# Kernel optimization log

Measured on AMD Instinct MI355X. Metric: run time of the kernel, lower is better.

Reference implementation:

```python
import jax, jax.numpy as jnp
import numpy as np
from jax import lax

R = 8  # REGION_NUM_

def _avgpool3(x):
    # AvgPool2d(kernel=H-2*(H//3), stride=H//3) -> exactly 3x3 spatial output
    H = x.shape[2]
    s = H // 3
    k = H - 2 * s
    y = lax.reduce_window(x, 0.0, lax.add, (1, 1, k, k), (1, 1, s, s), 'VALID')
    return y / float(k * k)

def _hist_drconv(x, hist, wa, ba, wb, bb, out_ch):
    # x: [B,Cin,H,W], hist: [B,R,H,W]
    B, Cin, H, W = x.shape
    p = _avgpool3(x)                                                     # [B,Cin,3,3]
    h = jax.nn.sigmoid(jnp.einsum('bchw,oc->bohw', p, wa) + ba[None, :, None, None])  # [B,R*R,3,3]
    hg = h.reshape(B, R, R, 3, 3)
    wbg = wb.reshape(R, Cin * out_ch, R)                                 # grouped 1x1 conv, groups=R
    kern = jnp.einsum('brchw,roc->brohw', hg, wbg) + bb.reshape(1, R, Cin * out_ch, 1, 1)
    ki = kern.reshape(B, R * out_ch, Cin, 3, 3)                          # per-sample dynamic kernels
    def per_sample(xi, kb):
        # xi: [Cin,H,W], kb: [R*out,Cin,3,3] -> [R*out,H,W]
        return lax.conv_general_dilated(xi[None], kb, (1, 1), [(1, 1), (1, 1)])[0]
    y = jax.vmap(per_sample)(x, ki)                                      # [B,R*out,H,W]
    y = y.reshape(B, R, out_ch, H, W)
    # asign_index: one-hot of argmax over regions, select-sum
    mask = jax.nn.one_hot(jnp.argmax(hist, axis=1), R, axis=1, dtype=y.dtype)  # [B,R,H,W]
    return (y * mask[:, :, None]).sum(axis=1)                            # [B,out,H,W]

def _bn_relu(y, g, b, m, v):
    scale = (g / jnp.sqrt(v + 1e-5))[None, :, None, None]
    return jax.nn.relu((y - m[None, :, None, None]) * scale + b[None, :, None, None])

def setup_inputs() -> dict:
    key = jax.random.key(0)
    ks = jax.random.split(key, 20)
    B, Cin, Cmid, Cout, H = 8, 8, 8, 8, 256
    f32 = jnp.float32
    d = {}
    d['x'] = jax.random.normal(ks[0], (B, Cin, H, H), f32)
    d['histmap'] = jax.random.uniform(ks[1], (B, R, H, H), dtype=f32)
    d['w1a'] = jax.random.normal(ks[2], (R * R, Cin), f32) * 0.1
    d['b1a'] = jax.random.normal(ks[3], (R * R,), f32) * 0.1
    d['w1b'] = jax.random.normal(ks[4], (R * Cin * Cmid, R), f32) * 0.1
    d['b1b'] = jax.random.normal(ks[5], (R * Cin * Cmid,), f32) * 0.1
    d['g1'] = jax.random.uniform(ks[6], (Cmid,), dtype=f32) + 0.5
    d['be1'] = jax.random.normal(ks[7], (Cmid,), f32) * 0.1
    d['m1'] = jax.random.normal(ks[8], (Cmid,), f32) * 0.1
    d['v1'] = jax.random.uniform(ks[9], (Cmid,), dtype=f32) + 0.5
    d['w2a'] = jax.random.normal(ks[10], (R * R, Cmid), f32) * 0.1
    d['b2a'] = jax.random.normal(ks[11], (R * R,), f32) * 0.1
    d['w2b'] = jax.random.normal(ks[12], (R * Cmid * Cout, R), f32) * 0.1
    d['b2b'] = jax.random.normal(ks[13], (R * Cmid * Cout,), f32) * 0.1
    d['g2'] = jax.random.uniform(ks[14], (Cout,), dtype=f32) + 0.5
    d['be2'] = jax.random.normal(ks[15], (Cout,), f32) * 0.1
    d['m2'] = jax.random.normal(ks[16], (Cout,), f32) * 0.1
    d['v2'] = jax.random.uniform(ks[17], (Cout,), dtype=f32) + 0.5
    return d

def reference(x, histmap, w1a, b1a, w1b, b1b, g1, be1, m1, v1,
              w2a, b2a, w2b, b2b, g2, be2, m2, v2):
    y = _hist_drconv(x, histmap, w1a, b1a, w1b, b1b, 8)
    y = _bn_relu(y, g1, be1, m1, v1)
    y = _hist_drconv(y, histmap, w2a, b2a, w2b, b2b, 8)
    return _bn_relu(y, g2, be2, m2, v2)
```

## Files before the change

kernel.cpp:

```cpp
#include <hip/hip_runtime.h>
#include <math.h>


#define HWPX 65536
#define HDIM 256

typedef __fp16 h2 __attribute__((ext_vector_type(2)));

#if defined(__has_builtin) && __has_builtin(__builtin_amdgcn_fdot2)
__device__ __forceinline__ float fdot2(h2 a, h2 b, float c) {
  return __builtin_amdgcn_fdot2(a, b, c, false);
}
#else
__device__ __forceinline__ float fdot2(h2 a, h2 b, float c) {
  return c + (float)a[0] * (float)b[0] + (float)a[1] * (float)b[1];
}
#endif

union UH { uint u; h2 h; };
union U4H { uint4 u4; h2 h[4]; };

__global__ __launch_bounds__(256) void prep_kernel(const float* __restrict__ x,
                                                   const float* __restrict__ hist,
                                                   float* __restrict__ rs1,
                                                   uint* __restrict__ xh,
                                                   unsigned char* __restrict__ regmap) {
  int u = blockIdx.x;
  int t = threadIdx.x;
  int wave = t >> 6, lane = t & 63;
  if (u < 2048) {
    int cp = u & 3, rg = (u >> 2) & 63, b = u >> 8;
    int row = rg * 4 + wave;
    const float* pa = x + ((size_t)(b * 8 + 2 * cp) * HWPX) + row * HDIM + lane * 4;
    const float4 va = *(const float4*)pa;
    const float4 vb = *(const float4*)(pa + HWPX);
    U4H pk;
    pk.h[0] = __builtin_amdgcn_cvt_pkrtz(va.x, vb.x);
    pk.h[1] = __builtin_amdgcn_cvt_pkrtz(va.y, vb.y);
    pk.h[2] = __builtin_amdgcn_cvt_pkrtz(va.z, vb.z);
    pk.h[3] = __builtin_amdgcn_cvt_pkrtz(va.w, vb.w);
    *(uint4*)(xh + (size_t)(b * 4 + cp) * HWPX + row * HDIM + lane * 4) = pk.u4;
    float a0 = 0.f, a1 = 0.f, a2 = 0.f, b0 = 0.f, b1 = 0.f, b2 = 0.f;
#pragma unroll
    for (int p = 0; p < 4; p++) {
      int px = lane * 4 + p;
      float fa = (&va.x)[p], fb = (&vb.x)[p];
      if (px <= 85)  { a0 += fa; b0 += fb; }
      if (px >= 85 && px <= 170) { a1 += fa; b1 += fb; }
      if (px >= 170) { a2 += fa; b2 += fb; }
    }
#pragma unroll
    for (int off = 32; off >= 1; off >>= 1) {
      a0 += __shfl_xor(a0, off); a1 += __shfl_xor(a1, off); a2 += __shfl_xor(a2, off);
      b0 += __shfl_xor(b0, off); b1 += __shfl_xor(b1, off); b2 += __shfl_xor(b2, off);
    }
    if (lane == 0) {
      float* qa = rs1 + ((size_t)(b * 8 + 2 * cp) * 256 + row) * 3;
      qa[0] = a0; qa[1] = a1; qa[2] = a2;
      float* qb = qa + 768;
      qb[0] = b0; qb[1] = b1; qb[2] = b2;
    }
  } else {
    int u2 = u - 2048;
    int b = u2 >> 6, rg = u2 & 63;
    int row = rg * 4 + wave;
    int x0 = lane * 4;
    const float* hp = hist + (size_t)b * 8 * HWPX + row * HDIM + x0;
    float4 hv[8];
#pragma unroll
    for (int r = 0; r < 8; r++) hv[r] = *(const float4*)(hp + (size_t)r * HWPX);
    uchar4 rg4;
#pragma unroll
    for (int p = 0; p < 4; p++) {
      float best = (&hv[0].x)[p];
      int reg = 0;
#pragma unroll
      for (int r = 1; r < 8; r++) {
        float q = (&hv[r].x)[p];
        if (q > best) { best = q; reg = r; }
      }
      (&rg4.x)[p] = (unsigned char)reg;
    }
    *(uchar4*)(regmap + (size_t)b * HWPX + row * HDIM + x0) = rg4;
  }
}

template <int LAYER>
__global__ __launch_bounds__(256) void conv_kernel(
    const uint* __restrict__ xh, const unsigned char* __restrict__ regmap,
    const float* __restrict__ rs,
    const float* __restrict__ wa, const float* __restrict__ ba,
    const float* __restrict__ wb, const float* __restrict__ bb,
    const float* __restrict__ g, const float* __restrict__ be,
    const float* __restrict__ m, const float* __restrict__ v,
    uint* __restrict__ outh, float* __restrict__ outf,
    float* __restrict__ rs2out) {
  __shared__ uint KsU[8 * 292];
  __shared__ float pp[72][3];
  __shared__ float pP[8][9];
  __shared__ float hh[576];
  __shared__ float bns[8], bnsh[8];

  int bid = blockIdx.x;
  int b = bid & 7;
  int rg = bid >> 3;
  int wave = threadIdx.x >> 6, lane = threadIdx.x & 63;
  int row = rg * 4 + wave;
  int x0 = lane * 4;
  int t = threadIdx.x;

  if (t < 216) {
    int u = t / 3, part = t - 3 * (t / 3);
    int c = u / 9, ij = u % 9, i = ij / 3, j = ij % 3;
    int r0 = 85 * i + part * 29;
    int cnt = (part == 2) ? 28 : 29;
    const float* q = rs + ((size_t)(b * 8 + c) * 256 + r0) * 3 + j;
    float s = 0.f;
    for (int k = 0; k < cnt; k++) s += q[k * 3];
    pp[u][part] = s;
  }
  if (t >= 248) {
    int oc = t - 248;
    float s = g[oc] * rsqrtf(v[oc] + 1e-5f);
    bns[oc] = s;
    bnsh[oc] = be[oc] - m[oc] * s;
  }
  __syncthreads();
  if (t < 72) pP[t / 9][t % 9] = (pp[t][0] + pp[t][1] + pp[t][2]) * (1.f / 7396.f);
  __syncthreads();
  for (int u = t; u < 576; u += 256) {
    int o = u / 9, ij = u - o * 9;
    float z = ba[o];
#pragma unroll
    for (int c = 0; c < 8; c++) z += pP[c][ij] * wa[o * 8 + c];
    hh[u] = 1.f / (1.f + expf(-z));
  }
  __syncthreads();
  {
    int reg = t >> 5, z = t & 31, oc = z >> 2, q = z & 3;
    int row0 = reg * 64 + oc * 8 + q * 2;
    const float* w0p = wb + row0 * 8;
    float4 wA  = *(const float4*)(w0p);
    float4 wA2 = *(const float4*)(w0p + 4);
    float4 wB  = *(const float4*)(w0p + 8);
    float4 wB2 = *(const float4*)(w0p + 12);
    float bb0 = bb[row0], bb1 = bb[row0 + 1];
    const float* hp = hh + reg * 72;
#pragma unroll
    for (int tap = 0; tap < 9; tap++) {
      float v0 = bb0, v1 = bb1;
#pragma unroll
      for (int cc = 0; cc < 4; cc++) {
        float hv = hp[cc * 9 + tap];
        v0 += hv * (&wA.x)[cc];
        v1 += hv * (&wB.x)[cc];
      }
#pragma unroll
      for (int cc = 0; cc < 4; cc++) {
        float hv = hp[(4 + cc) * 9 + tap];
        v0 += hv * (&wA2.x)[cc];
        v1 += hv * (&wB2.x)[cc];
      }
      UH pk;
      pk.h[0] = (__fp16)v0;
      pk.h[1] = (__fp16)v1;
      KsU[reg * 292 + tap * 32 + z] = pk.u;
    }
  }
  __syncthreads();

  uint win[4][3][6];
#pragma unroll
  for (int cp = 0; cp < 4; cp++) {
    const uint* plane = xh + (size_t)(b * 4 + cp) * HWPX;
#pragma unroll
    for (int dy = 0; dy < 3; dy++) {
      int yy = row + dy - 1;
      if ((unsigned)yy < 256u) {
        const uint* rp = plane + yy * HDIM + x0;
        uint4 mv = *(const uint4*)rp;
        win[cp][dy][0] = (x0 > 0) ? rp[-1] : 0u;
        win[cp][dy][1] = mv.x; win[cp][dy][2] = mv.y;
        win[cp][dy][3] = mv.z; win[cp][dy][4] = mv.w;
        win[cp][dy][5] = (x0 < 252) ? rp[4] : 0u;
      } else {
#pragma unroll
        for (int q = 0; q < 6; q++) win[cp][dy][q] = 0u;
      }
    }
  }

  uchar4 rg4 = *(const uchar4*)(regmap + (size_t)b * HWPX + row * HDIM + x0);

  float acc[4][8];
#pragma unroll
  for (int p = 0; p < 4; p++)
#pragma unroll
    for (int oc = 0; oc < 8; oc++) acc[p][oc] = 0.f;

#pragma unroll
  for (int p = 0; p < 4; p++) {
    int reg = (&rg4.x)[p];
    const char* Kr = (const char*)KsU + reg * 1168;
#pragma unroll
    for (int di = 0; di < 3; di++) {
#pragma unroll
      for (int dj = 0; dj < 3; dj++) {
        UH w0, w1, w2, w3;
        w0.u = win[0][di][p + dj];
        w1.u = win[1][di][p + dj];
        w2.u = win[2][di][p + dj];
        w3.u = win[3][di][p + dj];
        const char* kt = Kr + (di * 3 + dj) * 128;
#pragma unroll
        for (int oc = 0; oc < 8; oc++) {
          U4H kw;
          kw.u4 = *(const uint4*)(kt + oc * 16);
          float a = acc[p][oc];
          a = fdot2(w0.h, kw.h[0], a);
          a = fdot2(w1.h, kw.h[1], a);
          a = fdot2(w2.h, kw.h[2], a);
          a = fdot2(w3.h, kw.h[3], a);
          acc[p][oc] = a;
        }
      }
    }
  }

#pragma unroll
  for (int p = 0; p < 4; p++)
#pragma unroll
    for (int oc = 0; oc < 8; oc++)
      acc[p][oc] = fmaxf(acc[p][oc] * bns[oc] + bnsh[oc], 0.f);

  if (LAYER == 1) {
#pragma unroll
    for (int cp = 0; cp < 4; cp++) {
      U4H pk;
#pragma unroll
      for (int p = 0; p < 4; p++)
        pk.h[p] = __builtin_amdgcn_cvt_pkrtz(acc[p][2 * cp], acc[p][2 * cp + 1]);
      *(uint4*)(outh + (size_t)(b * 4 + cp) * HWPX + row * HDIM + x0) = pk.u4;
    }
#pragma unroll
    for (int oc = 0; oc < 8; oc++) {
      float s0 = 0.f, s1 = 0.f, s2 = 0.f;
#pragma unroll
      for (int p = 0; p < 4; p++) {
        int px = x0 + p;
        float val = acc[p][oc];
        if (px <= 85) s0 += val;
        if (px >= 85 && px <= 170) s1 += val;
        if (px >= 170) s2 += val;
      }
#pragma unroll
      for (int off = 32; off >= 1; off >>= 1) {
        s0 += __shfl_xor(s0, off);
        s1 += __shfl_xor(s1, off);
        s2 += __shfl_xor(s2, off);
      }
      if (lane == 0) {
        float* q = rs2out + ((size_t)(b * 8 + oc) * 256 + row) * 3;
        q[0] = s0; q[1] = s1; q[2] = s2;
      }
    }
  } else {
#pragma unroll
    for (int oc = 0; oc < 8; oc++) {
      float4 o4 = make_float4(acc[0][oc], acc[1][oc], acc[2][oc], acc[3][oc]);
      *(float4*)(outf + (size_t)(b * 8 + oc) * HWPX + row * HDIM + x0) = o4;
    }
  }
}

extern "C" void kernel_launch(void* const* d_in, const int* in_sizes, int n_in,
                              void* d_out, int out_size, void* d_ws, size_t ws_size,
                              hipStream_t stream) {
  const float* x    = (const float*)d_in[0];
  const float* hist = (const float*)d_in[1];
  const float* w1a  = (const float*)d_in[2];
  const float* b1a  = (const float*)d_in[3];
  const float* w1b  = (const float*)d_in[4];
  const float* b1b  = (const float*)d_in[5];
  const float* g1   = (const float*)d_in[6];
  const float* be1  = (const float*)d_in[7];
  const float* m1   = (const float*)d_in[8];
  const float* v1   = (const float*)d_in[9];
  const float* w2a  = (const float*)d_in[10];
  const float* b2a  = (const float*)d_in[11];
  const float* w2b  = (const float*)d_in[12];
  const float* b2b  = (const float*)d_in[13];
  const float* g2   = (const float*)d_in[14];
  const float* be2  = (const float*)d_in[15];
  const float* m2   = (const float*)d_in[16];
  const float* v2   = (const float*)d_in[17];
  float* outp = (float*)d_out;

  char* ws = (char*)d_ws;
  unsigned char* regmap = (unsigned char*)ws;
  uint* xh  = (uint*)(ws + 524288);
  uint* y1h = (uint*)(ws + 8912896);
  float* rs1 = (float*)(ws + 17301504);
  float* rs2 = (float*)(ws + 17399808);

  prep_kernel<<<2560, 256, 0, stream>>>(x, hist, rs1, xh, regmap);
  conv_kernel<1><<<512, 256, 0, stream>>>(xh, regmap, rs1, w1a, b1a, w1b, b1b,
                                          g1, be1, m1, v1, y1h, nullptr, rs2);
  conv_kernel<2><<<512, 256, 0, stream>>>(y1h, regmap, rs2, w2a, b2a, w2b, b2b,
                                          g2, be2, m2, v2, nullptr, outp, nullptr);
}
```

Before: 55.72 us.

## Fuse fp16 packing and region argmax into first conv kernel

The fp32-to-fp16 packing of x and the histogram argmax move out of the prep kernel into the first conv kernel, which now reads x and hist directly and writes the region map. The prep kernel shrinks to just the row-sum pass, removing the xh intermediate buffer round trip through memory. Global loads in conv1 are issued before the dynamic-kernel generation so they can overlap with it. The cost is that conv1 reads x as fp32, including halo rows, which is more traffic per block, and it carries more register pressure from the extra loads.

New measurement: 58.96 us. 1.06x slower.

```diff
diff --git a/kernel.cpp b/kernel.cpp
--- a/kernel.cpp
+++ b/kernel.cpp
@@ -20,81 +20,47 @@
 union UH { uint u; h2 h; };
 union U4H { uint4 u4; h2 h[4]; };
 
-__global__ __launch_bounds__(256) void prep_kernel(const float* __restrict__ x,
-                                                   const float* __restrict__ hist,
-                                                   float* __restrict__ rs1,
-                                                   uint* __restrict__ xh,
-                                                   unsigned char* __restrict__ regmap) {
+__global__ __launch_bounds__(256) void rowsum_kernel(const float* __restrict__ x,
+                                                     float* __restrict__ rs1) {
   int u = blockIdx.x;
   int t = threadIdx.x;
   int wave = t >> 6, lane = t & 63;
-  if (u < 2048) {
-    int cp = u & 3, rg = (u >> 2) & 63, b = u >> 8;
-    int row = rg * 4 + wave;
-    const float* pa = x + ((size_t)(b * 8 + 2 * cp) * HWPX) + row * HDIM + lane * 4;
-    const float4 va = *(const float4*)pa;
-    const float4 vb = *(const float4*)(pa + HWPX);
-    U4H pk;
-    pk.h[0] = __builtin_amdgcn_cvt_pkrtz(va.x, vb.x);
-    pk.h[1] = __builtin_amdgcn_cvt_pkrtz(va.y, vb.y);
-    pk.h[2] = __builtin_amdgcn_cvt_pkrtz(va.z, vb.z);
-    pk.h[3] = __builtin_amdgcn_cvt_pkrtz(va.w, vb.w);
-    *(uint4*)(xh + (size_t)(b * 4 + cp) * HWPX + row * HDIM + lane * 4) = pk.u4;
-    float a0 = 0.f, a1 = 0.f, a2 = 0.f, b0 = 0.f, b1 = 0.f, b2 = 0.f;
-#pragma unroll
-    for (int p = 0; p < 4; p++) {
-      int px = lane * 4 + p;
-      float fa = (&va.x)[p], fb = (&vb.x)[p];
-      if (px <= 85)  { a0 += fa; b0 += fb; }
-      if (px >= 85 && px <= 170) { a1 += fa; b1 += fb; }
-      if (px >= 170) { a2 += fa; b2 += fb; }
-    }
-#pragma unroll
-    for (int off = 32; off >= 1; off >>= 1) {
-      a0 += __shfl_xor(a0, off); a1 += __shfl_xor(a1, off); a2 += __shfl_xor(a2, off);
-      b0 += __shfl_xor(b0, off); b1 += __shfl_xor(b1, off); b2 += __shfl_xor(b2, off);
-    }
-    if (lane == 0) {
-      float* qa = rs1 + ((size_t)(b * 8 + 2 * cp) * 256 + row) * 3;
-      qa[0] = a0; qa[1] = a1; qa[2] = a2;
-      float* qb = qa + 768;
-      qb[0] = b0; qb[1] = b1; qb[2] = b2;
-    }
-  } else {
-    int u2 = u - 2048;
-    int b = u2 >> 6, rg = u2 & 63;
-    int row = rg * 4 + wave;
-    int x0 = lane * 4;
-    const float* hp = hist + (size_t)b * 8 * HWPX + row * HDIM + x0;
-    float4 hv[8];
-#pragma unroll
-    for (int r = 0; r < 8; r++) hv[r] = *(const float4*)(hp + (size_t)r * HWPX);
-    uchar4 rg4;
-#pragma unroll
-    for (int p = 0; p < 4; p++) {
-      float best = (&hv[0].x)[p];
-      int reg = 0;
-#pragma unroll
-      for (int r = 1; r < 8; r++) {
-        float q = (&hv[r].x)[p];
-        if (q > best) { best = q; reg = r; }
-      }
-      (&rg4.x)[p] = (unsigned char)reg;
-    }
-    *(uchar4*)(regmap + (size_t)b * HWPX + row * HDIM + x0) = rg4;
-  }
-}
-
-template <int LAYER>
-__global__ __launch_bounds__(256) void conv_kernel(
-    const uint* __restrict__ xh, const unsigned char* __restrict__ regmap,
+  int cp = u & 3, rg = (u >> 2) & 63, b = u >> 8;
+  int row = rg * 4 + wave;
+  const float* pa = x + ((size_t)(b * 8 + 2 * cp) * HWPX) + row * HDIM + lane * 4;
+  const float4 va = *(const float4*)pa;
+  const float4 vb = *(const float4*)(pa + HWPX);
+  float a0 = 0.f, a1 = 0.f, a2 = 0.f, b0 = 0.f, b1 = 0.f, b2 = 0.f;
+#pragma unroll
+  for (int p = 0; p < 4; p++) {
+    int px = lane * 4 + p;
+    float fa = (&va.x)[p], fb = (&vb.x)[p];
+    if (px <= 85)  { a0 += fa; b0 += fb; }
+    if (px >= 85 && px <= 170) { a1 += fa; b1 += fb; }
+    if (px >= 170) { a2 += fa; b2 += fb; }
+  }
+#pragma unroll
+  for (int off = 32; off >= 1; off >>= 1) {
+    a0 += __shfl_xor(a0, off); a1 += __shfl_xor(a1, off); a2 += __shfl_xor(a2, off);
+    b0 += __shfl_xor(b0, off); b1 += __shfl_xor(b1, off); b2 += __shfl_xor(b2, off);
+  }
+  if (lane == 0) {
+    float* qa = rs1 + ((size_t)(b * 8 + 2 * cp) * 256 + row) * 3;
+    qa[0] = a0; qa[1] = a1; qa[2] = a2;
+    float* qb = qa + 768;
+    qb[0] = b0; qb[1] = b1; qb[2] = b2;
+  }
+}
+
+__global__ __launch_bounds__(256) void conv1_kernel(
+    const float* __restrict__ x, const float* __restrict__ hist,
     const float* __restrict__ rs,
+    unsigned char* __restrict__ regmap,
     const float* __restrict__ wa, const float* __restrict__ ba,
     const float* __restrict__ wb, const float* __restrict__ bb,
     const float* __restrict__ g, const float* __restrict__ be,
     const float* __restrict__ m, const float* __restrict__ v,
-    uint* __restrict__ outh, float* __restrict__ outf,
-    float* __restrict__ rs2out) {
+    uint* __restrict__ outh, float* __restrict__ rs2out) {
   __shared__ uint KsU[8 * 292];
   __shared__ float pp[72][3];
   __shared__ float pP[8][9];
@@ -108,6 +74,57 @@
   int row = rg * 4 + wave;
   int x0 = lane * 4;
   int t = threadIdx.x;
+
+  uint win[4][3][6];
+#pragma unroll
+  for (int cp = 0; cp < 4; cp++) {
+    const float* pa = x + (size_t)(b * 8 + 2 * cp) * HWPX;
+    const float* pb = pa + HWPX;
+#pragma unroll
+    for (int dy = 0; dy < 3; dy++) {
+      int yy = row + dy - 1;
+      if ((unsigned)yy < 256u) {
+        const float* ra = pa + yy * HDIM + x0;
+        const float* rb = pb + yy * HDIM + x0;
+        float4 va = *(const float4*)ra;
+        float4 vb = *(const float4*)rb;
+        float al = (x0 > 0) ? ra[-1] : 0.f;
+        float bl = (x0 > 0) ? rb[-1] : 0.f;
+        float ar = (x0 < 252) ? ra[4] : 0.f;
+        float br = (x0 < 252) ? rb[4] : 0.f;
+        UH h;
+        h.h = __builtin_amdgcn_cvt_pkrtz(al, bl);     win[cp][dy][0] = h.u;
+        h.h = __builtin_amdgcn_cvt_pkrtz(va.x, vb.x); win[cp][dy][1] = h.u;
+        h.h = __builtin_amdgcn_cvt_pkrtz(va.y, vb.y); win[cp][dy][2] = h.u;
+        h.h = __builtin_amdgcn_cvt_pkrtz(va.z, vb.z); win[cp][dy][3] = h.u;
+        h.h = __builtin_amdgcn_cvt_pkrtz(va.w, vb.w); win[cp][dy][4] = h.u;
+        h.h = __builtin_amdgcn_cvt_pkrtz(ar, br);     win[cp][dy][5] = h.u;
+      } else {
+#pragma unroll
+        for (int q = 0; q < 6; q++) win[cp][dy][q] = 0u;
+      }
+    }
+  }
+
+  uchar4 rg4;
+  {
+    const float* hp = hist + (size_t)b * 8 * HWPX + row * HDIM + x0;
+    float4 hv[8];
+#pragma unroll
+    for (int r = 0; r < 8; r++) hv[r] = *(const float4*)(hp + (size_t)r * HWPX);
+#pragma unroll
+    for (int p = 0; p < 4; p++) {
+      float best = (&hv[0].x)[p];
+      int reg = 0;
+#pragma unroll
+      for (int r = 1; r < 8; r++) {
+        float q = (&hv[r].x)[p];
+        if (q > best) { best = q; reg = r; }
+      }
+      (&rg4.x)[p] = (unsigned char)reg;
+    }
+    *(uchar4*)(regmap + (size_t)b * HWPX + row * HDIM + x0) = rg4;
+  }
 
   if (t < 216) {
     int u = t / 3, part = t - 3 * (t / 3);
@@ -169,6 +186,101 @@
   }
   __syncthreads();
 
+  float acc[4][8];
+#pragma unroll
+  for (int p = 0; p < 4; p++)
+#pragma unroll
+    for (int oc = 0; oc < 8; oc++) acc[p][oc] = 0.f;
+
+#pragma unroll
+  for (int p = 0; p < 4; p++) {
+    int reg = (&rg4.x)[p];
+    const char* Kr = (const char*)KsU + reg * 1168;
+#pragma unroll
+    for (int di = 0; di < 3; di++) {
+#pragma unroll
+      for (int dj = 0; dj < 3; dj++) {
+        UH w0, w1, w2, w3;
+        w0.u = win[0][di][p + dj];
+        w1.u = win[1][di][p + dj];
+        w2.u = win[2][di][p + dj];
+        w3.u = win[3][di][p + dj];
+        const char* kt = Kr + (di * 3 + dj) * 128;
+#pragma unroll
+        for (int oc = 0; oc < 8; oc++) {
+          U4H kw;
+          kw.u4 = *(const uint4*)(kt + oc * 16);
+          float a = acc[p][oc];
+          a = fdot2(w0.h, kw.h[0], a);
+          a = fdot2(w1.h, kw.h[1], a);
+          a = fdot2(w2.h, kw.h[2], a);
+          a = fdot2(w3.h, kw.h[3], a);
+          acc[p][oc] = a;
+        }
+      }
+    }
+  }
+
+#pragma unroll
+  for (int p = 0; p < 4; p++)
+#pragma unroll
+    for (int oc = 0; oc < 8; oc++)
+      acc[p][oc] = fmaxf(acc[p][oc] * bns[oc] + bnsh[oc], 0.f);
+
+#pragma unroll
+  for (int cp = 0; cp < 4; cp++) {
+    U4H pk;
+#pragma unroll
+    for (int p = 0; p < 4; p++)
+      pk.h[p] = __builtin_amdgcn_cvt_pkrtz(acc[p][2 * cp], acc[p][2 * cp + 1]);
+    *(uint4*)(outh + (size_t)(b * 4 + cp) * HWPX + row * HDIM + x0) = pk.u4;
+  }
+#pragma unroll
+  for (int oc = 0; oc < 8; oc++) {
+    float s0 = 0.f, s1 = 0.f, s2 = 0.f;
+#pragma unroll
+    for (int p = 0; p < 4; p++) {
+      int px = x0 + p;
+      float val = acc[p][oc];
+      if (px <= 85) s0 += val;
+      if (px >= 85 && px <= 170) s1 += val;
+      if (px >= 170) s2 += val;
+    }
+#pragma unroll
+    for (int off = 32; off >= 1; off >>= 1) {
+      s0 += __shfl_xor(s0, off);
+      s1 += __shfl_xor(s1, off);
+      s2 += __shfl_xor(s2, off);
+    }
+    if (lane == 0) {
+      float* q = rs2out + ((size_t)(b * 8 + oc) * 256 + row) * 3;
+      q[0] = s0; q[1] = s1; q[2] = s2;
+    }
+  }
+}
+
+__global__ __launch_bounds__(256) void conv2_kernel(
+    const uint* __restrict__ xh, const unsigned char* __restrict__ regmap,
+    const float* __restrict__ rs,
+    const float* __restrict__ wa, const float* __restrict__ ba,
+    const float* __restrict__ wb, const float* __restrict__ bb,
+    const float* __restrict__ g, const float* __restrict__ be,
+    const float* __restrict__ m, const float* __restrict__ v,
+    float* __restrict__ outf) {
+  __shared__ uint KsU[8 * 292];
+  __shared__ float pp[72][3];
+  __shared__ float pP[8][9];
+  __shared__ float hh[576];
+  __shared__ float bns[8], bnsh[8];
+
+  int bid = blockIdx.x;
+  int b = bid & 7;
+  int rg = bid >> 3;
+  int wave = threadIdx.x >> 6, lane = threadIdx.x & 63;
+  int row = rg * 4 + wave;
+  int x0 = lane * 4;
+  int t = threadIdx.x;
+
   uint win[4][3][6];
 #pragma unroll
   for (int cp = 0; cp < 4; cp++) {
@@ -189,8 +301,67 @@
       }
     }
   }
-
   uchar4 rg4 = *(const uchar4*)(regmap + (size_t)b * HWPX + row * HDIM + x0);
+
+  if (t < 216) {
+    int u = t / 3, part = t - 3 * (t / 3);
+    int c = u / 9, ij = u % 9, i = ij / 3, j = ij % 3;
+    int r0 = 85 * i + part * 29;
+    int cnt = (part == 2) ? 28 : 29;
+    const float* q = rs + ((size_t)(b * 8 + c) * 256 + r0) * 3 + j;
+    float s = 0.f;
+    for (int k = 0; k < cnt; k++) s += q[k * 3];
+    pp[u][part] = s;
+  }
+  if (t >= 248) {
+    int oc = t - 248;
+    float s = g[oc] * rsqrtf(v[oc] + 1e-5f);
+    bns[oc] = s;
+    bnsh[oc] = be[oc] - m[oc] * s;
+  }
+  __syncthreads();
+  if (t < 72) pP[t / 9][t % 9] = (pp[t][0] + pp[t][1] + pp[t][2]) * (1.f / 7396.f);
+  __syncthreads();
+  for (int u = t; u < 576; u += 256) {
+    int o = u / 9, ij = u - o * 9;
+    float z = ba[o];
+#pragma unroll
+    for (int c = 0; c < 8; c++) z += pP[c][ij] * wa[o * 8 + c];
+    hh[u] = 1.f / (1.f + expf(-z));
+  }
+  __syncthreads();
+  {
+    int reg = t >> 5, z = t & 31, oc = z >> 2, q = z & 3;
+    int row0 = reg * 64 + oc * 8 + q * 2;
+    const float* w0p = wb + row0 * 8;
+    float4 wA  = *(const float4*)(w0p);
+    float4 wA2 = *(const float4*)(w0p + 4);
+    float4 wB  = *(const float4*)(w0p + 8);
+    float4 wB2 = *(const float4*)(w0p + 12);
+    float bb0 = bb[row0], bb1 = bb[row0 + 1];
+    const float* hp = hh + reg * 72;
+#pragma unroll
+    for (int tap = 0; tap < 9; tap++) {
+      float v0 = bb0, v1 = bb1;
+#pragma unroll
+      for (int cc = 0; cc < 4; cc++) {
+        float hv = hp[cc * 9 + tap];
+        v0 += hv * (&wA.x)[cc];
+        v1 += hv * (&wB.x)[cc];
+      }
+#pragma unroll
+      for (int cc = 0; cc < 4; cc++) {
+        float hv = hp[(4 + cc) * 9 + tap];
+        v0 += hv * (&wA2.x)[cc];
+        v1 += hv * (&wB2.x)[cc];
+      }
+      UH pk;
+      pk.h[0] = (__fp16)v0;
+      pk.h[1] = (__fp16)v1;
+      KsU[reg * 292 + tap * 32 + z] = pk.u;
+    }
+  }
+  __syncthreads();
 
   float acc[4][8];
 #pragma unroll
@@ -233,43 +404,10 @@
     for (int oc = 0; oc < 8; oc++)
       acc[p][oc] = fmaxf(acc[p][oc] * bns[oc] + bnsh[oc], 0.f);
 
-  if (LAYER == 1) {
-#pragma unroll
-    for (int cp = 0; cp < 4; cp++) {
-      U4H pk;
-#pragma unroll
-      for (int p = 0; p < 4; p++)
-        pk.h[p] = __builtin_amdgcn_cvt_pkrtz(acc[p][2 * cp], acc[p][2 * cp + 1]);
-      *(uint4*)(outh + (size_t)(b * 4 + cp) * HWPX + row * HDIM + x0) = pk.u4;
-    }
-#pragma unroll
-    for (int oc = 0; oc < 8; oc++) {
-      float s0 = 0.f, s1 = 0.f, s2 = 0.f;
-#pragma unroll
-      for (int p = 0; p < 4; p++) {
-        int px = x0 + p;
-        float val = acc[p][oc];
-        if (px <= 85) s0 += val;
-        if (px >= 85 && px <= 170) s1 += val;
-        if (px >= 170) s2 += val;
-      }
-#pragma unroll
-      for (int off = 32; off >= 1; off >>= 1) {
-        s0 += __shfl_xor(s0, off);
-        s1 += __shfl_xor(s1, off);
-        s2 += __shfl_xor(s2, off);
-      }
-      if (lane == 0) {
-        float* q = rs2out + ((size_t)(b * 8 + oc) * 256 + row) * 3;
-        q[0] = s0; q[1] = s1; q[2] = s2;
-      }
-    }
-  } else {
-#pragma unroll
-    for (int oc = 0; oc < 8; oc++) {
-      float4 o4 = make_float4(acc[0][oc], acc[1][oc], acc[2][oc], acc[3][oc]);
-      *(float4*)(outf + (size_t)(b * 8 + oc) * HWPX + row * HDIM + x0) = o4;
-    }
+#pragma unroll
+  for (int oc = 0; oc < 8; oc++) {
+    float4 o4 = make_float4(acc[0][oc], acc[1][oc], acc[2][oc], acc[3][oc]);
+    *(float4*)(outf + (size_t)(b * 8 + oc) * HWPX + row * HDIM + x0) = o4;
   }
 }
 
@@ -298,14 +436,15 @@
 
   char* ws = (char*)d_ws;
   unsigned char* regmap = (unsigned char*)ws;
-  uint* xh  = (uint*)(ws + 524288);
-  uint* y1h = (uint*)(ws + 8912896);
-  float* rs1 = (float*)(ws + 17301504);
-  float* rs2 = (float*)(ws + 17399808);
-
-  prep_kernel<<<2560, 256, 0, stream>>>(x, hist, rs1, xh, regmap);
-  conv_kernel<1><<<512, 256, 0, stream>>>(xh, regmap, rs1, w1a, b1a, w1b, b1b,
-                                          g1, be1, m1, v1, y1h, nullptr, rs2);
-  conv_kernel<2><<<512, 256, 0, stream>>>(y1h, regmap, rs2, w2a, b2a, w2b, b2b,
-                                          g2, be2, m2, v2, nullptr, outp, nullptr);
-}
+  uint* y1h = (uint*)(ws + 524288);
+  float* rs1 = (float*)(ws + 8912896);
+  float* rs2 = (float*)(ws + 9109504);
+
+  rowsum_kernel<<<2048, 256, 0, stream>>>(x, rs1);
+  conv1_kernel<<<512, 256, 0, stream>>>(x, hist, rs1, regmap,
+                                        w1a, b1a, w1b, b1b,
+                                        g1, be1, m1, v1, y1h, rs2);
+  conv2_kernel<<<512, 256, 0, stream>>>(y1h, regmap, rs2,
+                                        w2a, b2a, w2b, b2b,
+                                        g2, be2, m2, v2, outp);
+}
```
